# Kernel tuning notes

Measured on AMD Instinct MI355X. Metric: run time of the kernel, lower is better.

The kernel has to match this reference:

```python
import jax, jax.numpy as jnp
import numpy as np


def silu(x):
    return x * jax.nn.sigmoid(x)


def setup_inputs() -> dict:
    key = jax.random.key(0)
    ks = jax.random.split(key, 12)
    B, S, Dm = 2, 2048, 768
    I, N, R, K = 1536, 16, 48, 4
    s = 0.02
    return {
        "input_states": jax.random.normal(ks[0], (B, S, Dm), jnp.float32),
        "in_proj_w": jax.random.normal(ks[1], (2 * I, Dm), jnp.float32) * s,
        "conv_w": jax.random.normal(ks[2], (I, 1, K), jnp.float32) * s,
        "conv_b": jax.random.normal(ks[3], (I,), jnp.float32) * s,
        "x_proj_w": jax.random.normal(ks[4], (R + 2 * N, I), jnp.float32) * s,
        "dt_proj_w": jax.random.normal(ks[5], (I, R), jnp.float32) * s,
        "dt_proj_b": jax.random.normal(ks[6], (I,), jnp.float32) * s,
        "A_log": jax.random.normal(ks[7], (I, N), jnp.float32) * 0.5,
        "D": jax.random.normal(ks[8], (I,), jnp.float32) * s,
        "out_proj_w": jax.random.normal(ks[9], (Dm, I), jnp.float32) * s,
        "alpha": jax.random.uniform(ks[10], (I,), jnp.float32),
        "feature_gating": jax.random.uniform(ks[11], (I,), jnp.float32),
    }


def reference(input_states, in_proj_w, conv_w, conv_b, x_proj_w,
              dt_proj_w, dt_proj_b, A_log, D, out_proj_w,
              alpha, feature_gating):
    Bsz, S, _ = input_states.shape
    I, N = A_log.shape
    R = dt_proj_w.shape[1]
    K = conv_w.shape[-1]

    # in_proj (no bias), chunk into hidden / gate, each [B, I, S]
    proj = jnp.einsum('bsd,ed->bse', input_states, in_proj_w)  # [B, S, 2I]
    hidden, gate = jnp.split(proj.transpose(0, 2, 1), 2, axis=1)

    # causal depthwise conv1d + SiLU
    h = jax.lax.conv_general_dilated(
        hidden, conv_w, window_strides=(1,), padding=[(K - 1, 0)],
        dimension_numbers=('NCH', 'OIH', 'NCH'), feature_group_count=I)
    h = silu(h + conv_b[None, :, None])  # [B, I, S]

    # x_proj -> time_step, B, C
    ssm_p = jnp.einsum('bis,ei->bse', h, x_proj_w)  # [B, S, R+2N]
    ts, Bm, Cm = jnp.split(ssm_p, [R, R + N], axis=-1)

    dt = jax.nn.softplus(jnp.einsum('bsr,ir->bsi', ts, dt_proj_w) + dt_proj_b)
    dt = dt.transpose(0, 2, 1)                       # [B, I, S]
    dt = dt.at[:, :, -1].multiply(alpha[None, :])    # alpha scales last step

    A = -jnp.exp(A_log.astype(jnp.float32))          # [I, N]
    dA = jnp.exp(A[None, :, None, :] * dt[:, :, :, None])       # [B, I, S, N]
    dBu = dt[:, :, :, None] * Bm[:, None, :, :] * h[:, :, :, None]  # [B, I, S, N]

    def step(state, xs):
        dA_t, dBu_t, C_t = xs
        state = dA_t * state + dBu_t                 # [B, I, N]
        y = jnp.einsum('bin,bn->bi', state, C_t)
        return state, y

    init = jnp.zeros((Bsz, I, N), input_states.dtype)
    _, ys = jax.lax.scan(
        step, init,
        (dA.transpose(2, 0, 1, 3), dBu.transpose(2, 0, 1, 3), Cm.transpose(1, 0, 2)))
    y = ys.transpose(1, 2, 0)                        # [B, I, S]

    y = (y + h * D[None, :, None]) * silu(gate)
    y = y.at[:, :, -1].multiply(feature_gating[None, :])
    return jnp.einsum('bis,di->bsd', y, out_proj_w)  # [B, S, Dm]
```

## Files before the change

kernel.cpp:

```cpp
#include <hip/hip_runtime.h>
#include <math.h>


static constexpr int S_LEN  = 2048;
static constexpr int DMODEL = 768;
static constexpr int ICH    = 1536;
static constexpr int NST    = 16;
static constexpr int MROWS  = 4096;
static constexpr int NCH    = 64;
static constexpr int CHS    = 32;
static constexpr int CSTR   = 2 * ICH * NST;

typedef _Float16 f16;
typedef f16 f16x8 __attribute__((ext_vector_type(8)));
typedef f16 f16x4 __attribute__((ext_vector_type(4)));
typedef f16 f16x2 __attribute__((ext_vector_type(2)));
typedef float f32x4 __attribute__((ext_vector_type(4)));

#if __has_builtin(__builtin_amdgcn_exp2f)
#define EXP2F(x) __builtin_amdgcn_exp2f(x)
#else
#define EXP2F(x) exp2f(x)
#endif

typedef __attribute__((address_space(3))) void lds_void;
typedef const __attribute__((address_space(1))) void glb_void;

__device__ __forceinline__ void glds16(f16* l, const f16* g) {
    __builtin_amdgcn_global_load_lds((glb_void*)g, (lds_void*)l, 16, 0, 0);
}

__device__ __forceinline__ float silu_f(float x) {
    return x / (1.0f + __expf(-x));
}

__global__ __launch_bounds__(256) void cvt3(
    const float* __restrict__ s0, f16* __restrict__ d0, int n0,
    const float* __restrict__ s1, f16* __restrict__ d1, int n1,
    const float* __restrict__ s2, f16* __restrict__ d2)
{
    int i = (blockIdx.x * 256 + threadIdx.x) * 4;
    const float* s; f16* d;
    if (i < n0)            { s = s0 + i;            d = d0 + i; }
    else if (i < n0 + n1)  { s = s1 + (i - n0);     d = d1 + (i - n0); }
    else                   { s = s2 + (i - n0 - n1); d = d2 + (i - n0 - n1); }
    float4 v = *(const float4*)s;
    f16x4 o = { (f16)v.x, (f16)v.y, (f16)v.z, (f16)v.w };
    *(f16x4*)d = o;
}

__global__ __launch_bounds__(256) void k1m(
    const f16* __restrict__ Xh,
    const f16* __restrict__ Wh,
    f16* __restrict__ hidden,
    f16* __restrict__ sgate)
{
    __shared__ __align__(16) f16 As[2][128 * 32];
    __shared__ __align__(16) f16 Bs[2][64 * 32];
    const int tid = threadIdx.x;
    const int lane = tid & 63, wave = tid >> 6;
    const int quad = lane >> 4, l16 = lane & 15;
    const int wm = wave & 1, wn = wave >> 1;
    const int m0 = blockIdx.x * 128, n0 = blockIdx.y * 64;
    const int l_row = lane >> 2, l_c8 = (lane & 3) * 8;

    const f16* Ag = Xh + (size_t)(m0 + wave * 16 + l_row) * 768 + l_c8;
    const f16* Bg = Wh + (size_t)(n0 + wave * 16 + l_row) * 768 + l_c8;
    const int aLo = (wave * 16) * 32, aHi = (64 + wave * 16) * 32;
    const int bOff = (wave * 16) * 32;

#define K1_STAGE(buf, kk)                                        \
    do {                                                         \
        glds16(&As[buf][aLo], Ag + (kk));                        \
        glds16(&As[buf][aHi], Ag + (size_t)64 * 768 + (kk));     \
        glds16(&Bs[buf][bOff], Bg + (kk));                       \
    } while (0)

#define K1_COMPUTE(buf)                                                        \
    do {                                                                       \
        f16x8 af[4], bf[2];                                                    \
        _Pragma("unroll")                                                      \
        for (int mi = 0; mi < 4; ++mi)                                         \
            af[mi] = *(const f16x8*)&As[buf][(wm * 64 + mi * 16 + l16) * 32 + quad * 8]; \
        _Pragma("unroll")                                                      \
        for (int ni = 0; ni < 2; ++ni)                                         \
            bf[ni] = *(const f16x8*)&Bs[buf][(wn * 32 + ni * 16 + l16) * 32 + quad * 8]; \
        _Pragma("unroll")                                                      \
        for (int mi = 0; mi < 4; ++mi)                                         \
            _Pragma("unroll")                                                  \
            for (int ni = 0; ni < 2; ++ni)                                     \
                acc[mi][ni] = __builtin_amdgcn_mfma_f32_16x16x32_f16(          \
                    af[mi], bf[ni], acc[mi][ni], 0, 0, 0);                     \
    } while (0)

    K1_STAGE(0, 0);
    __syncthreads();

    f32x4 acc[4][2] = {};
    for (int k0 = 0; k0 < 768; k0 += 64) {
        K1_STAGE(1, k0 + 32);
        K1_COMPUTE(0);
        __syncthreads();
        if (k0 + 64 < 768) K1_STAGE(0, k0 + 64);
        K1_COMPUTE(1);
        __syncthreads();
    }
#undef K1_STAGE
#undef K1_COMPUTE

    const bool isGate = (n0 >= ICH);
    f16* outp = isGate ? sgate : hidden;
    const int e0 = (isGate ? (n0 - ICH) : n0) + wn * 32 + l16;
    #pragma unroll
    for (int mi = 0; mi < 4; ++mi) {
        #pragma unroll
        for (int ni = 0; ni < 2; ++ni) {
            #pragma unroll
            for (int r = 0; r < 4; ++r) {
                int m = m0 + wm * 64 + mi * 16 + quad * 4 + r;
                int e = e0 + ni * 16;
                float v = acc[mi][ni][r];
                if (isGate) v = silu_f(v);
                outp[(size_t)m * ICH + e] = (f16)v;
            }
        }
    }
}

__global__ __launch_bounds__(256) void k3m(
    const f16* __restrict__ hidden,
    const float* __restrict__ conv_w,
    const float* __restrict__ conv_b,
    const float* __restrict__ xw,
    f16* __restrict__ h,
    float* __restrict__ ssmp)
{
    __shared__ __align__(16) f16 Ah[128 * 32];
    __shared__ __align__(16) f16 Bh[80 * 32];
    __shared__ float4 cwv[96];
    __shared__ float  cbv[96];
    const int tid = threadIdx.x;
    const int lane = tid & 63, wave = tid >> 6;
    const int quad = lane >> 4, l16 = lane & 15;
    const int m0 = blockIdx.x * 128;
    const int kbeg = blockIdx.y * 96;

    if (tid < 96) {
        cwv[tid] = *(const float4*)(conv_w + (size_t)(kbeg + tid) * 4);
        cbv[tid] = conv_b[kbeg + tid];
    }

    f32x4 acc[2][5] = {};
    for (int k0 = kbeg; k0 < kbeg + 96; k0 += 32) {
        __syncthreads();
        #pragma unroll
        for (int it = 0; it < 2; ++it) {
            int slot = tid + it * 256;
            int r_ = slot >> 2, c_ = (slot & 3) * 8;
            int gm = m0 + r_, c = k0 + c_;
            int s = gm & (S_LEN - 1);
            const f16* bp = hidden + (size_t)gm * ICH + c;
            f16x8 x0 = *(const f16x8*)bp;
            f16x8 x1 = *(const f16x8*)(bp - (s >= 1 ? ICH : 0));
            f16x8 x2 = *(const f16x8*)(bp - (s >= 2 ? 2 * ICH : 0));
            f16x8 x3 = *(const f16x8*)(bp - (s >= 3 ? 3 * ICH : 0));
            f16x8 o;
            #pragma unroll
            for (int j = 0; j < 8; ++j) {
                int ci = (k0 - kbeg) + c_ + j;
                float4 w = cwv[ci];
                float v1 = (s >= 1) ? (float)x1[j] : 0.f;
                float v2 = (s >= 2) ? (float)x2[j] : 0.f;
                float v3 = (s >= 3) ? (float)x3[j] : 0.f;
                float r = cbv[ci] + w.x * v3 + w.y * v2 + w.z * v1 + w.w * (float)x0[j];
                o[j] = (f16)silu_f(r);
            }
            *(f16x8*)&Ah[r_ * 32 + c_] = o;
            *(f16x8*)(h + (size_t)gm * ICH + c) = o;
        }
        {
            int c4 = (tid & 7) * 4;
            for (int r = tid >> 3; r < 80; r += 32) {
                float4 v = *(const float4*)(xw + (size_t)r * ICH + k0 + c4);
                f16x4 o = { (f16)v.x, (f16)v.y, (f16)v.z, (f16)v.w };
                *(f16x4*)&Bh[r * 32 + c4] = o;
            }
        }
        __syncthreads();
        f16x8 af[2], bf[5];
        #pragma unroll
        for (int mi = 0; mi < 2; ++mi)
            af[mi] = *(const f16x8*)&Ah[(wave * 32 + mi * 16 + l16) * 32 + quad * 8];
        #pragma unroll
        for (int j = 0; j < 5; ++j)
            bf[j] = *(const f16x8*)&Bh[(j * 16 + l16) * 32 + quad * 8];
        #pragma unroll
        for (int mi = 0; mi < 2; ++mi)
            #pragma unroll
            for (int j = 0; j < 5; ++j)
                acc[mi][j] = __builtin_amdgcn_mfma_f32_16x16x32_f16(
                    af[mi], bf[j], acc[mi][j], 0, 0, 0);
    }
    #pragma unroll
    for (int mi = 0; mi < 2; ++mi) {
        #pragma unroll
        for (int j = 0; j < 5; ++j) {
            #pragma unroll
            for (int r = 0; r < 4; ++r) {
                int m = m0 + wave * 32 + mi * 16 + quad * 4 + r;
                atomicAdd(ssmp + (size_t)m * 80 + j * 16 + l16, acc[mi][j][r]);
            }
        }
    }
}

__global__ __launch_bounds__(256) void k4m(
    const float* __restrict__ ssmp,
    const float* __restrict__ dtw,
    const float* __restrict__ dtb,
    const float* __restrict__ alpha,
    f16* __restrict__ dt)
{
    __shared__ __align__(16) f16 As[128 * 72];
    __shared__ __align__(16) f16 Bs[128 * 72];
    const int tid = threadIdx.x;
    const int lane = tid & 63, wave = tid >> 6;
    const int quad = lane >> 4, l16 = lane & 15;
    const int wm = wave & 1, wn = wave >> 1;
    const int m0 = blockIdx.x * 128, n0 = blockIdx.y * 128;
    const int srow = tid >> 1;
    const int shalf = tid & 1;

    {
        const float* sa = ssmp + (size_t)(m0 + srow) * 80 + shalf * 24;
        const float* sb = dtw + (size_t)(n0 + srow) * 48 + shalf * 24;
        f16* da = &As[srow * 72 + shalf * 24];
        f16* db = &Bs[srow * 72 + shalf * 24];
        #pragma unroll
        for (int j = 0; j < 6; ++j) {
            float4 va = *(const float4*)(sa + 4 * j);
            float4 vb = *(const float4*)(sb + 4 * j);
            f16x4 oa = { (f16)va.x, (f16)va.y, (f16)va.z, (f16)va.w };
            f16x4 ob = { (f16)vb.x, (f16)vb.y, (f16)vb.z, (f16)vb.w };
            *(f16x4*)(da + 4 * j) = oa;
            *(f16x4*)(db + 4 * j) = ob;
        }
        if (shalf) {
            f16x8 z = {};
            *(f16x8*)&As[srow * 72 + 48] = z;
            *(f16x8*)&As[srow * 72 + 56] = z;
            *(f16x8*)&Bs[srow * 72 + 48] = z;
            *(f16x8*)&Bs[srow * 72 + 56] = z;
        }
    }
    __syncthreads();

    f32x4 acc[4][4] = {};
    #pragma unroll
    for (int ks = 0; ks < 2; ++ks) {
        f16x8 af[4], bf[4];
        #pragma unroll
        for (int mi = 0; mi < 4; ++mi)
            af[mi] = *(const f16x8*)&As[(wm * 64 + mi * 16 + l16) * 72 + ks * 32 + quad * 8];
        #pragma unroll
        for (int ni = 0; ni < 4; ++ni)
            bf[ni] = *(const f16x8*)&Bs[(wn * 64 + ni * 16 + l16) * 72 + ks * 32 + quad * 8];
        #pragma unroll
        for (int mi = 0; mi < 4; ++mi)
            #pragma unroll
            for (int ni = 0; ni < 4; ++ni)
                acc[mi][ni] = __builtin_amdgcn_mfma_f32_16x16x32_f16(
                    af[mi], bf[ni], acc[mi][ni], 0, 0, 0);
    }

    #pragma unroll
    for (int ni = 0; ni < 4; ++ni) {
        int e = n0 + wn * 64 + ni * 16 + l16;
        float bias = dtb[e];
        float al = alpha[e];
        #pragma unroll
        for (int mi = 0; mi < 4; ++mi) {
            #pragma unroll
            for (int r = 0; r < 4; ++r) {
                int m = m0 + wm * 64 + mi * 16 + quad * 4 + r;
                float x = acc[mi][ni][r] + bias;
                float sp = (x > 20.0f) ? x : __logf(1.0f + __expf(x));
                if ((m & (S_LEN - 1)) == S_LEN - 1) sp *= al;
                dt[(size_t)m * ICH + e] = (f16)sp;
            }
        }
    }
}

__global__ __launch_bounds__(256) void k5a_chunk(
    const f16* __restrict__ dt,
    const f16* __restrict__ h,
    const float* __restrict__ ssmp,
    const float* __restrict__ A_log,
    float* __restrict__ PArr,
    float* __restrict__ SfArr)
{
    __shared__ float dts[CHS * 64];
    __shared__ float hs[CHS * 64];
    __shared__ float Bc[CHS][16];
    const int tid = threadIdx.x;
    const int n4 = tid & 3;
    const int il = tid >> 2;
    const int i0 = blockIdx.x * 64;
    const int i = i0 + il;
    const int c = blockIdx.y;
    const int b = blockIdx.z;
    const int s0 = c * CHS;
    const size_t row0 = (size_t)(b * S_LEN + s0) * ICH + i0;

    #pragma unroll
    for (int k = 0; k < (CHS * 64) / 512; ++k) {
        int idx = (tid + k * 256) * 2;
        size_t g_off = row0 + (size_t)(idx >> 6) * ICH + (idx & 63);
        f16x2 dv = *(const f16x2*)(dt + g_off);
        f16x2 hv = *(const f16x2*)(h + g_off);
        dts[idx] = (float)dv[0]; dts[idx + 1] = (float)dv[1];
        hs[idx]  = (float)hv[0]; hs[idx + 1]  = (float)hv[1];
    }
    if (tid < CHS * 4) {
        int t = tid >> 2, q = tid & 3;
        *(float4*)&Bc[t][q * 4] =
            *(const float4*)(ssmp + (size_t)(b * S_LEN + s0 + t) * 80 + 48 + q * 4);
    }

    const float L2E = 1.44269504088896f;
    float4 alv = *(const float4*)(A_log + i * NST + n4 * 4);
    float A[4] = { -__expf(alv.x) * L2E, -__expf(alv.y) * L2E,
                   -__expf(alv.z) * L2E, -__expf(alv.w) * L2E };
    float st[4] = {};
    float cdt = 0.f;
    __syncthreads();
    #pragma unroll 4
    for (int t = 0; t < CHS; ++t) {
        float dtv = dts[t * 64 + il];
        float hv  = hs[t * 64 + il];
        float4 Bv = *(const float4*)&Bc[t][n4 * 4];
        cdt += dtv;
        float x = dtv * hv;
        #pragma unroll
        for (int j = 0; j < 4; ++j) {
            float dA = EXP2F(A[j] * dtv);
            st[j] = fmaf(dA, st[j], x * (&Bv.x)[j]);
        }
    }
    size_t base = (size_t)c * CSTR + (size_t)(b * ICH + i) * NST + n4 * 4;
    float4 Pv = { EXP2F(A[0] * cdt), EXP2F(A[1] * cdt),
                  EXP2F(A[2] * cdt), EXP2F(A[3] * cdt) };
    float4 Sv = { st[0], st[1], st[2], st[3] };
    *(float4*)(PArr + base)  = Pv;
    *(float4*)(SfArr + base) = Sv;
}

__global__ __launch_bounds__(256) void k5b_carry(
    const float* PArr,
    const float* __restrict__ SfArr,
    float* CIn)
{
    int idx = blockIdx.x * 256 + threadIdx.x;
    float p[NCH], s[NCH];
    #pragma unroll
    for (int c = 0; c < NCH; ++c) {
        size_t a = (size_t)c * CSTR + idx;
        p[c] = PArr[a];
        s[c] = SfArr[a];
    }
    float carry = 0.f;
    #pragma unroll
    for (int c = 0; c < NCH; ++c) {
        CIn[(size_t)c * CSTR + idx] = carry;
        carry = fmaf(p[c], carry, s[c]);
    }
}

__global__ __launch_bounds__(256) void k5c_emit(
    const f16* __restrict__ dt,
    const f16* __restrict__ h,
    const f16* __restrict__ sgate,
    const float* __restrict__ ssmp,
    const float* __restrict__ A_log,
    const float* __restrict__ Dp,
    const float* __restrict__ fg,
    const float* __restrict__ CIn,
    f16* __restrict__ yh)
{
    __shared__ float dts[CHS * 64];
    __shared__ float hs[CHS * 64];
    __shared__ float gs[CHS * 64];
    __shared__ float BC[CHS][32];
    const int tid = threadIdx.x;
    const int n4 = tid & 3;
    const int il = tid >> 2;
    const int i0 = blockIdx.x * 64;
    const int i = i0 + il;
    const int c = blockIdx.y;
    const int b = blockIdx.z;
    const int s0 = c * CHS;
    const size_t row0 = (size_t)(b * S_LEN + s0) * ICH + i0;

    #pragma unroll
    for (int k = 0; k < (CHS * 64) / 512; ++k) {
        int idx = (tid + k * 256) * 2;
        size_t g_off = row0 + (size_t)(idx >> 6) * ICH + (idx & 63);
        f16x2 dv = *(const f16x2*)(dt + g_off);
        f16x2 v = *(const f16x2*)(h + g_off);
        f16x2 w = *(const f16x2*)(sgate + g_off);
        dts[idx] = (float)dv[0]; dts[idx + 1] = (float)dv[1];
        hs[idx] = (float)v[0]; hs[idx + 1] = (float)v[1];
        gs[idx] = (float)w[0]; gs[idx + 1] = (float)w[1];
    }
    {
        int t = tid >> 3, q = tid & 7;
        *(float4*)&BC[t][q * 4] =
            *(const float4*)(ssmp + (size_t)(b * S_LEN + s0 + t) * 80 + 48 + q * 4);
    }

    const float L2E = 1.44269504088896f;
    float4 alv = *(const float4*)(A_log + i * NST + n4 * 4);
    float A[4] = { -__expf(alv.x) * L2E, -__expf(alv.y) * L2E,
                   -__expf(alv.z) * L2E, -__expf(alv.w) * L2E };
    const float Dv = Dp[i];
    const float fgv = fg[i];
    float4 civ = *(const float4*)(CIn + (size_t)c * CSTR + (size_t)(b * ICH + i) * NST + n4 * 4);
    float st[4] = { civ.x, civ.y, civ.z, civ.w };
    f16* yout = yh + row0 + il;
    const bool last_chunk = (c == NCH - 1);
    __syncthreads();
    #pragma unroll 4
    for (int t = 0; t < CHS; ++t) {
        float dtv = dts[t * 64 + il];
        float hv  = hs[t * 64 + il];
        float4 Bv = *(const float4*)&BC[t][n4 * 4];
        float4 Cv = *(const float4*)&BC[t][16 + n4 * 4];
        float x = dtv * hv;
        float yp = 0.f;
        #pragma unroll
        for (int j = 0; j < 4; ++j) {
            float dA = EXP2F(A[j] * dtv);
            st[j] = fmaf(dA, st[j], x * (&Bv.x)[j]);
            yp = fmaf(st[j], (&Cv.x)[j], yp);
        }
        yp += __shfl_xor(yp, 1, 4);
        yp += __shfl_xor(yp, 2, 4);
        if (n4 == 0) {
            float yv = fmaf(hv, Dv, yp) * gs[t * 64 + il];
            if (last_chunk && t == CHS - 1) yv *= fgv;
            yout[(size_t)t * ICH] = (f16)yv;
        }
    }
}

__global__ __launch_bounds__(256) void k6m(
    const f16* __restrict__ Yh,
    const f16* __restrict__ Wh,
    float* __restrict__ out)
{
    __shared__ __align__(16) f16 As[2][64 * 32];
    __shared__ __align__(16) f16 Bs[2][64 * 32];
    const int tid = threadIdx.x;
    const int lane = tid & 63, wave = tid >> 6;
    const int quad = lane >> 4, l16 = lane & 15;
    const int wm = wave & 1, wn = wave >> 1;
    const int m0 = blockIdx.x * 64, n0 = blockIdx.y * 64;
    const int l_row = lane >> 2, l_c8 = (lane & 3) * 8;

    const f16* Ag = Yh + (size_t)(m0 + wave * 16 + l_row) * ICH + l_c8;
    const f16* Bg = Wh + (size_t)(n0 + wave * 16 + l_row) * ICH + l_c8;
    const int aOff = (wave * 16) * 32;

#define K6_STAGE(buf, kk)                                        \
    do {                                                         \
        glds16(&As[buf][aOff], Ag + (kk));                       \
        glds16(&Bs[buf][aOff], Bg + (kk));                       \
    } while (0)

#define K6_COMPUTE(buf)                                                        \
    do {                                                                       \
        f16x8 af[2], bf[2];                                                    \
        _Pragma("unroll")                                                      \
        for (int mi = 0; mi < 2; ++mi)                                         \
            af[mi] = *(const f16x8*)&As[buf][(wm * 32 + mi * 16 + l16) * 32 + quad * 8]; \
        _Pragma("unroll")                                                      \
        for (int ni = 0; ni < 2; ++ni)                                         \
            bf[ni] = *(const f16x8*)&Bs[buf][(wn * 32 + ni * 16 + l16) * 32 + quad * 8]; \
        _Pragma("unroll")                                                      \
        for (int mi = 0; mi < 2; ++mi)                                         \
            _Pragma("unroll")                                                  \
            for (int ni = 0; ni < 2; ++ni)                                     \
                acc[mi][ni] = __builtin_amdgcn_mfma_f32_16x16x32_f16(          \
                    af[mi], bf[ni], acc[mi][ni], 0, 0, 0);                     \
    } while (0)

    K6_STAGE(0, 0);
    __syncthreads();

    f32x4 acc[2][2] = {};
    for (int k0 = 0; k0 < ICH; k0 += 64) {
        K6_STAGE(1, k0 + 32);
        K6_COMPUTE(0);
        __syncthreads();
        if (k0 + 64 < ICH) K6_STAGE(0, k0 + 64);
        K6_COMPUTE(1);
        __syncthreads();
    }
#undef K6_STAGE
#undef K6_COMPUTE

    #pragma unroll
    for (int mi = 0; mi < 2; ++mi) {
        #pragma unroll
        for (int ni = 0; ni < 2; ++ni) {
            #pragma unroll
            for (int r = 0; r < 4; ++r) {
                int m = m0 + wm * 32 + mi * 16 + quad * 4 + r;
                int d = n0 + wn * 32 + ni * 16 + l16;
                out[(size_t)m * DMODEL + d] = acc[mi][ni][r];
            }
        }
    }
}

extern "C" void kernel_launch(void* const* d_in, const int* in_sizes, int n_in,
                              void* d_out, int out_size, void* d_ws, size_t ws_size,
                              hipStream_t stream) {
    const float* X     = (const float*)d_in[0];
    const float* W1    = (const float*)d_in[1];
    const float* CW    = (const float*)d_in[2];
    const float* CB    = (const float*)d_in[3];
    const float* XW    = (const float*)d_in[4];
    const float* DTW   = (const float*)d_in[5];
    const float* DTB   = (const float*)d_in[6];
    const float* ALOG  = (const float*)d_in[7];
    const float* DD    = (const float*)d_in[8];
    const float* OW    = (const float*)d_in[9];
    const float* ALPHA = (const float*)d_in[10];
    const float* FG    = (const float*)d_in[11];
    float* out = (float*)d_out;

    const size_t NBI = (size_t)MROWS * ICH;
    f16* hidden_h = (f16*)d_ws;
    f16* sgate_h  = hidden_h + NBI;
    f16* h_h      = sgate_h + NBI;
    f16* dt_h     = h_h + NBI;
    float* ssmp   = (float*)(dt_h + NBI);
    f16* Xh       = (f16*)(ssmp + (size_t)MROWS * 80);
    f16* W1h      = Xh + (size_t)MROWS * DMODEL;
    f16* OWh      = W1h + (size_t)2 * ICH * DMODEL;
    float* SfA    = (float*)(OWh + (size_t)DMODEL * ICH);
    float* PArr = (float*)hidden_h;
    float* CIn  = PArr;
    f16* yh     = (f16*)SfA;

    const int nX = MROWS * DMODEL, nW1 = 2 * ICH * DMODEL, nOW = DMODEL * ICH;
    hipMemsetAsync(ssmp, 0, (size_t)MROWS * 80 * sizeof(float), stream);
    cvt3<<<dim3((nX + nW1 + nOW) / 1024), 256, 0, stream>>>(X, Xh, nX, W1, W1h, nW1, OW, OWh);
    k1m<<<dim3(32, 48), 256, 0, stream>>>(Xh, W1h, hidden_h, sgate_h);
    k3m<<<dim3(32, 16), 256, 0, stream>>>(hidden_h, CW, CB, XW, h_h, ssmp);
    k4m<<<dim3(32, 12), 256, 0, stream>>>(ssmp, DTW, DTB, ALPHA, dt_h);
    k5a_chunk<<<dim3(24, NCH, 2), 256, 0, stream>>>(dt_h, h_h, ssmp, ALOG, PArr, SfA);
    k5b_carry<<<dim3(192), 256, 0, stream>>>(PArr, SfA, CIn);
    k5c_emit<<<dim3(24, NCH, 2), 256, 0, stream>>>(dt_h, h_h, sgate_h, ssmp, ALOG, DD, FG, CIn, yh);
    k6m<<<dim3(64, 12), 256, 0, stream>>>(yh, OWh, out);
}
```

Before: 243.1 us.

## Fuse chunked scan passes into one cooperative kernel with grid syncs

Merges the three scan kernels (chunk summary, carry propagation, emit) into a single cooperative kernel that uses grid.sync between phases. dt and h are loaded into LDS only once, as f16 via direct global-to-LDS copies, and reused by both scan passes. Chunk size grows to 128, giving 16 chunks and 768 blocks. This removes two launches and the second global reload of dt/h, at the cost of grid-wide barriers, a serial carry phase that runs on only 192 of the blocks, and longer sequential chunks. It also requires all 768 blocks to be co-resident, which the launch bounds of 3 blocks per CU are meant to allow.

```diff
diff --git a/kernel.cpp b/kernel.cpp
--- a/kernel.cpp
+++ b/kernel.cpp
@@ -1,5 +1,8 @@
 #include <hip/hip_runtime.h>
+#include <hip/hip_cooperative_groups.h>
 #include <math.h>
+
+namespace cg = cooperative_groups;
 
 
 static constexpr int S_LEN  = 2048;
@@ -7,8 +10,8 @@
 static constexpr int ICH    = 1536;
 static constexpr int NST    = 16;
 static constexpr int MROWS  = 4096;
-static constexpr int NCH    = 64;
-static constexpr int CHS    = 32;
+static constexpr int NCH    = 16;
+static constexpr int CHS    = 128;
 static constexpr int CSTR   = 2 * ICH * NST;
 
 typedef _Float16 f16;
@@ -292,18 +295,24 @@
     }
 }
 
-__global__ __launch_bounds__(256) void k5a_chunk(
+__global__ __launch_bounds__(256, 3) void k5f(
     const f16* __restrict__ dt,
     const f16* __restrict__ h,
+    const f16* __restrict__ sgate,
     const float* __restrict__ ssmp,
     const float* __restrict__ A_log,
+    const float* __restrict__ Dp,
+    const float* __restrict__ fg,
     float* __restrict__ PArr,
-    float* __restrict__ SfArr)
+    float* __restrict__ SfArr,
+    float* __restrict__ CIn,
+    f16* __restrict__ yh)
 {
-    __shared__ float dts[CHS * 64];
-    __shared__ float hs[CHS * 64];
-    __shared__ float Bc[CHS][16];
+    __shared__ __align__(16) f16 dts[CHS * 64];
+    __shared__ __align__(16) f16 hs[CHS * 64];
+    __shared__ float BC[CHS][32];
     const int tid = threadIdx.x;
+    const int lane = tid & 63, wave = tid >> 6;
     const int n4 = tid & 3;
     const int il = tid >> 2;
     const int i0 = blockIdx.x * 64;
@@ -313,18 +322,19 @@
     const int s0 = c * CHS;
     const size_t row0 = (size_t)(b * S_LEN + s0) * ICH + i0;
 
+    {
+        const int gr = lane >> 3, gc = (lane & 7) * 8;
+        #pragma unroll
+        for (int j = 0; j < 4; ++j) {
+            const size_t go = row0 + (size_t)(wave * 32 + j * 8 + gr) * ICH + gc;
+            glds16(dts + wave * 2048 + j * 512, dt + go);
+            glds16(hs  + wave * 2048 + j * 512, h  + go);
+        }
+    }
     #pragma unroll
-    for (int k = 0; k < (CHS * 64) / 512; ++k) {
-        int idx = (tid + k * 256) * 2;
-        size_t g_off = row0 + (size_t)(idx >> 6) * ICH + (idx & 63);
-        f16x2 dv = *(const f16x2*)(dt + g_off);
-        f16x2 hv = *(const f16x2*)(h + g_off);
-        dts[idx] = (float)dv[0]; dts[idx + 1] = (float)dv[1];
-        hs[idx]  = (float)hv[0]; hs[idx + 1]  = (float)hv[1];
-    }
-    if (tid < CHS * 4) {
-        int t = tid >> 2, q = tid & 3;
-        *(float4*)&Bc[t][q * 4] =
+    for (int it = 0; it < 4; ++it) {
+        int t = (tid >> 3) + it * 32, q = tid & 7;
+        *(float4*)&BC[t][q * 4] =
             *(const float4*)(ssmp + (size_t)(b * S_LEN + s0 + t) * 80 + 48 + q * 4);
     }
 
@@ -332,124 +342,86 @@
     float4 alv = *(const float4*)(A_log + i * NST + n4 * 4);
     float A[4] = { -__expf(alv.x) * L2E, -__expf(alv.y) * L2E,
                    -__expf(alv.z) * L2E, -__expf(alv.w) * L2E };
-    float st[4] = {};
-    float cdt = 0.f;
     __syncthreads();
-    #pragma unroll 4
-    for (int t = 0; t < CHS; ++t) {
-        float dtv = dts[t * 64 + il];
-        float hv  = hs[t * 64 + il];
-        float4 Bv = *(const float4*)&Bc[t][n4 * 4];
-        cdt += dtv;
-        float x = dtv * hv;
-        #pragma unroll
-        for (int j = 0; j < 4; ++j) {
-            float dA = EXP2F(A[j] * dtv);
-            st[j] = fmaf(dA, st[j], x * (&Bv.x)[j]);
-        }
-    }
-    size_t base = (size_t)c * CSTR + (size_t)(b * ICH + i) * NST + n4 * 4;
-    float4 Pv = { EXP2F(A[0] * cdt), EXP2F(A[1] * cdt),
-                  EXP2F(A[2] * cdt), EXP2F(A[3] * cdt) };
-    float4 Sv = { st[0], st[1], st[2], st[3] };
-    *(float4*)(PArr + base)  = Pv;
-    *(float4*)(SfArr + base) = Sv;
-}
-
-__global__ __launch_bounds__(256) void k5b_carry(
-    const float* PArr,
-    const float* __restrict__ SfArr,
-    float* CIn)
-{
-    int idx = blockIdx.x * 256 + threadIdx.x;
-    float p[NCH], s[NCH];
-    #pragma unroll
-    for (int c = 0; c < NCH; ++c) {
-        size_t a = (size_t)c * CSTR + idx;
-        p[c] = PArr[a];
-        s[c] = SfArr[a];
-    }
-    float carry = 0.f;
-    #pragma unroll
-    for (int c = 0; c < NCH; ++c) {
-        CIn[(size_t)c * CSTR + idx] = carry;
-        carry = fmaf(p[c], carry, s[c]);
-    }
-}
-
-__global__ __launch_bounds__(256) void k5c_emit(
-    const f16* __restrict__ dt,
-    const f16* __restrict__ h,
-    const f16* __restrict__ sgate,
-    const float* __restrict__ ssmp,
-    const float* __restrict__ A_log,
-    const float* __restrict__ Dp,
-    const float* __restrict__ fg,
-    const float* __restrict__ CIn,
-    f16* __restrict__ yh)
-{
-    __shared__ float dts[CHS * 64];
-    __shared__ float hs[CHS * 64];
-    __shared__ float gs[CHS * 64];
-    __shared__ float BC[CHS][32];
-    const int tid = threadIdx.x;
-    const int n4 = tid & 3;
-    const int il = tid >> 2;
-    const int i0 = blockIdx.x * 64;
-    const int i = i0 + il;
-    const int c = blockIdx.y;
-    const int b = blockIdx.z;
-    const int s0 = c * CHS;
-    const size_t row0 = (size_t)(b * S_LEN + s0) * ICH + i0;
-
-    #pragma unroll
-    for (int k = 0; k < (CHS * 64) / 512; ++k) {
-        int idx = (tid + k * 256) * 2;
-        size_t g_off = row0 + (size_t)(idx >> 6) * ICH + (idx & 63);
-        f16x2 dv = *(const f16x2*)(dt + g_off);
-        f16x2 v = *(const f16x2*)(h + g_off);
-        f16x2 w = *(const f16x2*)(sgate + g_off);
-        dts[idx] = (float)dv[0]; dts[idx + 1] = (float)dv[1];
-        hs[idx] = (float)v[0]; hs[idx + 1] = (float)v[1];
-        gs[idx] = (float)w[0]; gs[idx + 1] = (float)w[1];
-    }
+
     {
-        int t = tid >> 3, q = tid & 7;
-        *(float4*)&BC[t][q * 4] =
-            *(const float4*)(ssmp + (size_t)(b * S_LEN + s0 + t) * 80 + 48 + q * 4);
-    }
-
-    const float L2E = 1.44269504088896f;
-    float4 alv = *(const float4*)(A_log + i * NST + n4 * 4);
-    float A[4] = { -__expf(alv.x) * L2E, -__expf(alv.y) * L2E,
-                   -__expf(alv.z) * L2E, -__expf(alv.w) * L2E };
-    const float Dv = Dp[i];
-    const float fgv = fg[i];
-    float4 civ = *(const float4*)(CIn + (size_t)c * CSTR + (size_t)(b * ICH + i) * NST + n4 * 4);
-    float st[4] = { civ.x, civ.y, civ.z, civ.w };
-    f16* yout = yh + row0 + il;
-    const bool last_chunk = (c == NCH - 1);
-    __syncthreads();
-    #pragma unroll 4
-    for (int t = 0; t < CHS; ++t) {
-        float dtv = dts[t * 64 + il];
-        float hv  = hs[t * 64 + il];
-        float4 Bv = *(const float4*)&BC[t][n4 * 4];
-        float4 Cv = *(const float4*)&BC[t][16 + n4 * 4];
-        float x = dtv * hv;
-        float yp = 0.f;
-        #pragma unroll
-        for (int j = 0; j < 4; ++j) {
-            float dA = EXP2F(A[j] * dtv);
-            st[j] = fmaf(dA, st[j], x * (&Bv.x)[j]);
-            yp = fmaf(st[j], (&Cv.x)[j], yp);
-        }
-        yp += __shfl_xor(yp, 1, 4);
-        yp += __shfl_xor(yp, 2, 4);
-        if (n4 == 0) {
-            float yv = fmaf(hv, Dv, yp) * gs[t * 64 + il];
-            if (last_chunk && t == CHS - 1) yv *= fgv;
-            yout[(size_t)t * ICH] = (f16)yv;
+        float st[4] = {};
+        float cdt = 0.f;
+        #pragma unroll 4
+        for (int t = 0; t < CHS; ++t) {
+            float dtv = (float)dts[t * 64 + il];
+            float hv  = (float)hs[t * 64 + il];
+            float4 Bv = *(const float4*)&BC[t][n4 * 4];
+            cdt += dtv;
+            float x = dtv * hv;
+            #pragma unroll
+            for (int j = 0; j < 4; ++j) {
+                float dA = EXP2F(A[j] * dtv);
+                st[j] = fmaf(dA, st[j], x * (&Bv.x)[j]);
+            }
+        }
+        size_t base = (size_t)c * CSTR + (size_t)(b * ICH + i) * NST + n4 * 4;
+        float4 Pv = { EXP2F(A[0] * cdt), EXP2F(A[1] * cdt),
+                      EXP2F(A[2] * cdt), EXP2F(A[3] * cdt) };
+        float4 Sv = { st[0], st[1], st[2], st[3] };
+        *(float4*)(PArr + base)  = Pv;
+        *(float4*)(SfArr + base) = Sv;
+    }
+
+    cg::grid_group grid = cg::this_grid();
+    grid.sync();
+
+    {
+        int lb = blockIdx.x + 24 * (blockIdx.y + 16 * blockIdx.z);
+        if (lb < 192) {
+            int idx = lb * 256 + tid;
+            float p[NCH], s[NCH];
+            #pragma unroll
+            for (int cc = 0; cc < NCH; ++cc) {
+                size_t a = (size_t)cc * CSTR + idx;
+                p[cc] = PArr[a];
+                s[cc] = SfArr[a];
+            }
+            float carry = 0.f;
+            #pragma unroll
+            for (int cc = 0; cc < NCH; ++cc) {
+                CIn[(size_t)cc * CSTR + idx] = carry;
+                carry = fmaf(p[cc], carry, s[cc]);
+            }
+        }
+    }
+
+    grid.sync();
+
+    {
+        const float Dv = Dp[i];
+        const float fgv = fg[i];
+        float4 civ = *(const float4*)(CIn + (size_t)c * CSTR + (size_t)(b * ICH + i) * NST + n4 * 4);
+        float st[4] = { civ.x, civ.y, civ.z, civ.w };
+        f16* yout = yh + row0 + il;
+        const bool last_chunk = (c == NCH - 1);
+        #pragma unroll 4
+        for (int t = 0; t < CHS; ++t) {
+            float dtv = (float)dts[t * 64 + il];
+            float hv  = (float)hs[t * 64 + il];
+            float4 Bv = *(const float4*)&BC[t][n4 * 4];
+            float4 Cv = *(const float4*)&BC[t][16 + n4 * 4];
+            float x = dtv * hv;
+            float yp = 0.f;
+            #pragma unroll
+            for (int j = 0; j < 4; ++j) {
+                float dA = EXP2F(A[j] * dtv);
+                st[j] = fmaf(dA, st[j], x * (&Bv.x)[j]);
+                yp = fmaf(st[j], (&Cv.x)[j], yp);
+            }
+            yp += __shfl_xor(yp, 1, 4);
+            yp += __shfl_xor(yp, 2, 4);
+            if (n4 == 0) {
+                float gv = (float)sgate[row0 + (size_t)t * ICH + il];
+                float yv = fmaf(hv, Dv, yp) * gv;
+                if (last_chunk && t == CHS - 1) yv *= fgv;
+                yout[(size_t)t * ICH] = (f16)yv;
+            }
         }
     }
 }
@@ -546,14 +518,14 @@
     f16* sgate_h  = hidden_h + NBI;
     f16* h_h      = sgate_h + NBI;
     f16* dt_h     = h_h + NBI;
-    float* ssmp   = (float*)(dt_h + NBI);
-    f16* Xh       = (f16*)(ssmp + (size_t)MROWS * 80);
+    f16* yh       = dt_h + NBI;
+    f16* Xh       = yh + NBI;
     f16* W1h      = Xh + (size_t)MROWS * DMODEL;
     f16* OWh      = W1h + (size_t)2 * ICH * DMODEL;
-    float* SfA    = (float*)(OWh + (size_t)DMODEL * ICH);
-    float* PArr = (float*)hidden_h;
-    float* CIn  = PArr;
-    f16* yh     = (f16*)SfA;
+    float* ssmp   = (float*)(OWh + (size_t)DMODEL * ICH);
+    float* PArr   = ssmp + (size_t)MROWS * 80;
+    float* SfArr  = PArr + (size_t)NCH * CSTR;
+    float* CIn    = SfArr + (size_t)NCH * CSTR;
 
     const int nX = MROWS * DMODEL, nW1 = 2 * ICH * DMODEL, nOW = DMODEL * ICH;
     hipMemsetAsync(ssmp, 0, (size_t)MROWS * 80 * sizeof(float), stream);
@@ -561,8 +533,12 @@
     k1m<<<dim3(32, 48), 256, 0, stream>>>(Xh, W1h, hidden_h, sgate_h);
     k3m<<<dim3(32, 16), 256, 0, stream>>>(hidden_h, CW, CB, XW, h_h, ssmp);
     k4m<<<dim3(32, 12), 256, 0, stream>>>(ssmp, DTW, DTB, ALPHA, dt_h);
-    k5a_chunk<<<dim3(24, NCH, 2), 256, 0, stream>>>(dt_h, h_h, ssmp, ALOG, PArr, SfA);
-    k5b_carry<<<dim3(192), 256, 0, stream>>>(PArr, SfA, CIn);
-    k5c_emit<<<dim3(24, NCH, 2), 256, 0, stream>>>(dt_h, h_h, sgate_h, ssmp, ALOG, DD, FG, CIn, yh);
+    {
+        void* args[] = { (void*)&dt_h, (void*)&h_h, (void*)&sgate_h, (void*)&ssmp,
+                         (void*)&ALOG, (void*)&DD, (void*)&FG,
+                         (void*)&PArr, (void*)&SfArr, (void*)&CIn, (void*)&yh };
+        hipLaunchCooperativeKernel((const void*)k5f, dim3(24, NCH, 2), dim3(256),
+                                   args, 0, stream);
+    }
     k6m<<<dim3(64, 12), 256, 0, stream>>>(yh, OWh, out);
 }
```

Result: slower. 451.4 us (+85.7%).
